# Performance work log

Hardware: AMD Instinct MI355X
Metric: run time of the kernel (lower is better)

The kernel has to match this reference:

```python
import jax, jax.numpy as jnp
import numpy as np

D_MODEL = 768
KERNELS = [7, 5, 3]
FILTERS = [40, 30, 20]
FC_IN = sum(FILTERS)  # 90


def setup_inputs() -> dict:
    key = jax.random.key(0)
    ks = jax.random.split(key, 16)
    B, S, D = 8, 2048, D_MODEL
    inp = {
        'x1': jax.random.normal(ks[0], (B, S, D), jnp.float32),
        'x2': jax.random.normal(ks[1], (B, S, D), jnp.float32),
    }
    # conv weights: OIH layout [out_ch, in_ch, k]
    for i, (k, f) in enumerate(zip(KERNELS, FILTERS)):
        scale = 1.0 / np.sqrt(D * k)
        inp[f'w{k}'] = jax.random.uniform(ks[2 + 2 * i], (f, D, k), jnp.float32, -scale, scale)
        inp[f'b{k}'] = jax.random.uniform(ks[3 + 2 * i], (f,), jnp.float32, -scale, scale)
    inp['U'] = jax.random.normal(ks[8], (D, D), jnp.float32) * (1.0 / np.sqrt(D))
    inp['bias_v'] = jax.random.normal(ks[9], (D,), jnp.float32) * 0.02
    inp['fc_w'] = jax.random.normal(ks[10], (D, FC_IN), jnp.float32) * (1.0 / np.sqrt(FC_IN))
    inp['fc_b'] = jnp.zeros((D,), jnp.float32)
    inp['fcx_w'] = jax.random.normal(ks[11], (D, 2 * D), jnp.float32) * (1.0 / np.sqrt(2 * D))
    inp['fcx_b'] = jnp.zeros((D,), jnp.float32)
    return inp


def _conv1d_same(x_ncs, w_oik, b_o, k):
    # x: [B, C, S], w: [O, C, k] -> [B, O, S], 'same' padding = k//2
    y = jax.lax.conv_general_dilated(
        x_ncs, w_oik, window_strides=(1,), padding=[(k // 2, k // 2)],
        dimension_numbers=('NCH', 'OIH', 'NCH'))
    return y + b_o[None, :, None]


def reference(x1, x2, w7, b7, w5, b5, w3, b3, U, bias_v, fc_w, fc_b, fcx_w, fcx_b):
    # CNN branch over x2 (dropout layers are identity in eval mode)
    xc = jnp.transpose(x2, (0, 2, 1))  # [B, D, S]
    feats = jnp.concatenate([
        jnp.transpose(_conv1d_same(xc, w7, b7, 7), (0, 2, 1)),
        jnp.transpose(_conv1d_same(xc, w5, b5, 5), (0, 2, 1)),
        jnp.transpose(_conv1d_same(xc, w3, b3, 3), (0, 2, 1)),
    ], axis=-1)                                    # [B, S, 90]
    x = jnp.tanh(jax.nn.relu(feats) @ fc_w.T + fc_b)  # [B, S, D]
    # biaffine attention: x1 @ U @ x2^T + x2 @ bias (broadcast over rows)
    attn = jnp.einsum('bsd,de,bte->bst', x1, U, x2) + (x2 @ bias_v)[:, None, :]
    attn = jax.nn.softmax(attn, axis=-1)           # [B, S, S]
    out = jnp.tanh(attn @ x2)                      # [B, S, D]
    x = x + out
    return jnp.concatenate([x1, x], axis=-1) @ fcx_w.T + fcx_b  # [B, S, D]
```

## Files before the change

### kernel.cpp

```cpp
#include <hip/hip_runtime.h>
#include <cmath>

#define D_MODEL 768
#define SEQ 2048
#define BATCH 8
#define FC_PAD 96
#define FC_PAD2 128
#define KCOMB (7 * D_MODEL)
#define KCHUNK 2688

typedef unsigned short ushort_t;
typedef _Float16 half_t;
typedef __attribute__((ext_vector_type(8))) _Float16 f16x8;
typedef __attribute__((ext_vector_type(8))) unsigned short u16x8;
typedef __attribute__((ext_vector_type(4))) unsigned short u16x4;
typedef __attribute__((ext_vector_type(4))) float f32x4;

struct Ptr8 { const ushort_t* p[8]; };

__device__ __forceinline__ ushort_t f2h(float x) {
    half_t h = (half_t)x;
    return __builtin_bit_cast(ushort_t, h);
}
__device__ __forceinline__ float h2f(ushort_t u) {
    return (float)__builtin_bit_cast(half_t, u);
}
__device__ __forceinline__ float fast_tanh(float x) {
    float a = fabsf(x);
    float t = __expf(-2.f * a);
    float r = (1.f - t) / (1.f + t);
    return copysignf(r, x);
}
__device__ __forceinline__ void gload16(const ushort_t* g, ushort_t* lbase) {
    __builtin_amdgcn_global_load_lds((const __attribute__((address_space(1))) void*)g,
                                     (__attribute__((address_space(3))) void*)lbase,
                                     16, 0, 0);
}

__global__ void convert_f16_kernel(const float* __restrict__ src, ushort_t* __restrict__ dst, size_t n4) {
    size_t i = (size_t)blockIdx.x * 256 + threadIdx.x;
    if (i >= n4) return;
    f32x4 x = *(const f32x4*)(src + i * 4);
    u16x4 h;
    #pragma unroll
    for (int j = 0; j < 4; ++j) h[j] = f2h(x[j]);
    *(u16x4*)(dst + i * 4) = h;
}

__global__ void convert_fc_kernel(const float* __restrict__ src, ushort_t* __restrict__ dst) {
    int i = blockIdx.x * 256 + threadIdx.x;
    if (i >= D_MODEL * FC_PAD2) return;
    int o = i / FC_PAD2, j = i - o * FC_PAD2;
    dst[i] = (j < 90) ? f2h(src[o * 90 + j]) : 0;
}

__global__ void convert_ut_kernel(const float* __restrict__ U, ushort_t* __restrict__ dst) {
    int i = blockIdx.x * 256 + threadIdx.x;
    if (i >= D_MODEL * D_MODEL) return;
    int n = i / D_MODEL, k = i - n * D_MODEL;
    dst[i] = f2h(U[(size_t)k * D_MODEL + n]);
}

__global__ void build_wcomb_kernel(const float* __restrict__ w7, const float* __restrict__ b7,
                                   const float* __restrict__ w5, const float* __restrict__ b5,
                                   const float* __restrict__ w3, const float* __restrict__ b3,
                                   ushort_t* __restrict__ Wt, float* __restrict__ bcat) {
    int idx = blockIdx.x * 256 + threadIdx.x;
    const int total = FC_PAD2 * KCOMB;
    if (idx < total) {
        int o = idx / KCOMB, k = idx - o * KCOMB;
        int t = k / D_MODEL, d = k - t * D_MODEL;
        float v = 0.f;
        if (o < 40) {
            v = w7[(size_t)o * (D_MODEL * 7) + d * 7 + t];
        } else if (o < 70) {
            int t5 = t - 1;
            if (t5 >= 0 && t5 < 5) v = w5[(size_t)(o - 40) * (D_MODEL * 5) + d * 5 + t5];
        } else if (o < 90) {
            int t3 = t - 2;
            if (t3 >= 0 && t3 < 3) v = w3[(size_t)(o - 70) * (D_MODEL * 3) + d * 3 + t3];
        }
        Wt[idx] = f2h(v);
    }
    if (idx < FC_PAD2) {
        float bv = 0.f;
        if (idx < 40) bv = b7[idx];
        else if (idx < 70) bv = b5[idx - 40];
        else if (idx < 90) bv = b3[idx - 70];
        bcat[idx] = bv;
    }
}

__global__ void conv_reduce_kernel(const float* __restrict__ P, const float* __restrict__ bcat,
                                   ushort_t* __restrict__ feats) {
    const size_t MT = (size_t)BATCH * SEQ;
    size_t i = (size_t)blockIdx.x * 256 + threadIdx.x;
    if (i >= MT * FC_PAD2) return;
    int col = (int)(i & (FC_PAD2 - 1));
    size_t row = i >> 7;
    float v = 0.f;
    if (col < FC_PAD) {
        size_t idx = row * FC_PAD + col;
        const size_t st = MT * FC_PAD;
        v = P[idx] + P[idx + st] + bcat[col];
        v = fmaxf(v, 0.f);
    }
    feats[i] = f2h(v);
}

__global__ void transpose_f16_kernel(const ushort_t* __restrict__ in, ushort_t* __restrict__ out) {
    __shared__ ushort_t tile[32][40];
    int b = blockIdx.z;
    int s0 = blockIdx.x * 32, d0 = blockIdx.y * 32;
    int tx = threadIdx.x & 31, ty = threadIdx.x >> 5;
    const ushort_t* inb = in + (size_t)b * SEQ * D_MODEL;
    ushort_t* outb = out + (size_t)b * D_MODEL * SEQ;
    #pragma unroll
    for (int i = 0; i < 4; ++i)
        tile[ty + i * 8][tx] = inb[(size_t)(s0 + ty + i * 8) * D_MODEL + d0 + tx];
    __syncthreads();
    #pragma unroll
    for (int i = 0; i < 4; ++i)
        outb[(size_t)(d0 + ty + i * 8) * SEQ + s0 + tx] = tile[tx][ty + i * 8];
}

template<int TM, int TN, int AMODE, int ACT, int HASBIAS, int HASADD,
         int OUTMODE, int KSPLIT, int APTR, int MAP, int ZM, int GX, int GY,
         int SMEPI, int ASCALE>
__global__ __launch_bounds__(256, 3)
void mfma_gemm(const ushort_t* __restrict__ A, const ushort_t* __restrict__ A2,
               const ushort_t* __restrict__ B, const float* __restrict__ bias,
               const ushort_t* __restrict__ addsrc,
               float* __restrict__ Cf, ushort_t* __restrict__ Ch,
               Ptr8 ap, float* __restrict__ smw, float* __restrict__ slw,
               int M, int N, int K, int lda, int ldb, int ldc,
               size_t sA, size_t sB, size_t sBias, size_t sC) {
    constexpr int WM = TM / 2, WN = TN / 2, FM = WM / 16, FN = WN / 16;
    __shared__ __align__(16) ushort_t As_[TM * 64];
    __shared__ __align__(16) ushort_t Bs_[TN * 64];
    __shared__ float pmS[SMEPI ? 4 : 1][SMEPI ? 64 : 1];
    __shared__ float msS[SMEPI ? 128 : 1];
    __shared__ float plS[SMEPI ? 4 : 1][SMEPI ? 64 : 1];
    __shared__ ushort_t alS[ASCALE ? 16 : 1][ASCALE ? 128 : 1];

    int bx, by, z;
    if (MAP == 1) {
        int lin = blockIdx.x;
        z = lin % ZM;
        int t = lin / ZM;
        bx = t % GX;
        by = t / GX;
    } else if (MAP == 2) {
        int lin = blockIdx.x;
        int xcd = lin & 7;
        int t = lin >> 3;
        by = t % GY;
        bx = xcd * (GX / 8) + t / GY;
        z = 0;
    } else if (MAP == 3) {
        int lin = blockIdx.x;
        z = lin % ZM;
        int t = lin / ZM;
        by = t % GY;
        bx = t / GY;
    } else {
        bx = blockIdx.x; by = blockIdx.y; z = blockIdx.z;
    }

    const int kb = KSPLIT ? z * K : 0;
    const ushort_t* Ab = APTR ? ap.p[z] : (A + (KSPLIT ? 0 : (size_t)z * sA));
    const ushort_t* Bb = B + (KSPLIT ? 0 : (size_t)z * sB);
    if (HASBIAS) bias += (size_t)z * sBias;
    if (HASADD) addsrc += (size_t)z * sC;
    if (OUTMODE == 0) Cf += (size_t)z * sC;
    else if (!SMEPI) Ch += (size_t)z * sC;

    const int m0 = bx * TM;
    const int n0 = by * TN;
    const int tid = threadIdx.x;
    const int lane = tid & 63;
    const int wave = tid >> 6;
    const int wm = (wave >> 1) * WM, wn = (wave & 1) * WN;
    const int r16 = lane & 15, kq = lane >> 4;
    const int srow = tid >> 3;
    const int slot = tid & 7;

    if (ASCALE) {
        if (tid < 128) {
            int row = tid;
            int gm = m0 + row;
            float mt[16], al[16];
            float mg = -3.0e38f;
            #pragma unroll
            for (int t = 0; t < 16; ++t) {
                mt[t] = smw[((size_t)z * 16 + t) * SEQ + gm];
                mg = fmaxf(mg, mt[t]);
            }
            float lg = 0.f;
            #pragma unroll
            for (int t = 0; t < 16; ++t) {
                float e = __expf(mt[t] - mg);
                lg += slw[((size_t)z * 16 + t) * SEQ + gm] * e;
                al[t] = e;
            }
            float inv = 1.f / lg;
            #pragma unroll
            for (int t = 0; t < 16; ++t) alS[t][row] = f2h(al[t] * inv);
        }
        __syncthreads();
    }

    f32x4 acc[FM][FN];
    #pragma unroll
    for (int i = 0; i < FM; ++i)
        #pragma unroll
        for (int j = 0; j < FN; ++j) acc[i][j] = (f32x4){0.f, 0.f, 0.f, 0.f};

    const u16x8 zv = {0, 0, 0, 0, 0, 0, 0, 0};

    for (int k0 = 0; k0 < K; k0 += 64) {
        #pragma unroll
        for (int i = 0; i < TM / 32; ++i) {
            int row = i * 32 + srow;
            int gm = m0 + row;
            int xs = slot ^ (row & 7);
            if (AMODE == 1) {
                int gkk = kb + k0 + xs * 8;
                int t = gkk / D_MODEL, d = gkk - t * D_MODEL;
                int s = (gm & (SEQ - 1)) + t - 3;
                int bb = gm >> 11;
                u16x8 v = (s >= 0 && s < SEQ) ? *(const u16x8*)(Ab + ((size_t)(bb * SEQ + s)) * lda + d) : zv;
                *(u16x8*)&As_[(size_t)row * 64 + slot * 8] = v;
            } else {
                const ushort_t* src;
                if (AMODE == 2) {
                    int gk = k0 + xs * 8;
                    src = (gk < D_MODEL) ? Ab + (size_t)gm * D_MODEL + gk
                                         : A2 + (size_t)gm * D_MODEL + (gk - D_MODEL);
                } else {
                    int gk = kb + k0 + xs * 8;
                    src = Ab + (size_t)gm * lda + gk;
                }
                gload16(src, &As_[(size_t)(i * 32 + wave * 8) * 64]);
            }
        }
        #pragma unroll
        for (int i = 0; i < TN / 32; ++i) {
            int row = i * 32 + srow;
            int gn = n0 + row;
            int xs = slot ^ (row & 7);
            int gk = kb + k0 + xs * 8;
            gload16(Bb + (size_t)gn * ldb + gk, &Bs_[(size_t)(i * 32 + wave * 8) * 64]);
        }
        __syncthreads();

        f16x8 ah[FM][2], bh[FN][2];
        #pragma unroll
        for (int mi = 0; mi < FM; ++mi) {
            int row = wm + mi * 16 + r16;
            #pragma unroll
            for (int kk = 0; kk < 2; ++kk)
                ah[mi][kk] = *(const f16x8*)&As_[(size_t)row * 64 + (((kk * 4 + kq) ^ (row & 7)) * 8)];
        }
        if (ASCALE) {
            const int kt = k0 >> 7;
            #pragma unroll
            for (int mi = 0; mi < FM; ++mi) {
                half_t s = __builtin_bit_cast(half_t, alS[kt][wm + mi * 16 + r16]);
                ah[mi][0] = ah[mi][0] * s;
                ah[mi][1] = ah[mi][1] * s;
            }
        }
        #pragma unroll
        for (int ni = 0; ni < FN; ++ni) {
            int row = wn + ni * 16 + r16;
            #pragma unroll
            for (int kk = 0; kk < 2; ++kk)
                bh[ni][kk] = *(const f16x8*)&Bs_[(size_t)row * 64 + (((kk * 4 + kq) ^ (row & 7)) * 8)];
        }
        #pragma unroll
        for (int kk = 0; kk < 2; ++kk)
            #pragma unroll
            for (int mi = 0; mi < FM; ++mi)
                #pragma unroll
                for (int ni = 0; ni < FN; ++ni)
                    acc[mi][ni] = __builtin_amdgcn_mfma_f32_16x16x32_f16(ah[mi][kk], bh[ni][kk], acc[mi][ni], 0, 0, 0);
        __syncthreads();
    }

    if (SMEPI) {
        float pmax[FM][4];
        #pragma unroll
        for (int mi = 0; mi < FM; ++mi)
            #pragma unroll
            for (int r = 0; r < 4; ++r) {
                float mx = -3.0e38f;
                #pragma unroll
                for (int ni = 0; ni < FN; ++ni) {
                    float v = acc[mi][ni][r];
                    if (HASBIAS) { v += bias[n0 + wn + ni * 16 + r16]; acc[mi][ni][r] = v; }
                    mx = fmaxf(mx, v);
                }
                mx = fmaxf(mx, __shfl_xor(mx, 1));
                mx = fmaxf(mx, __shfl_xor(mx, 2));
                mx = fmaxf(mx, __shfl_xor(mx, 4));
                mx = fmaxf(mx, __shfl_xor(mx, 8));
                pmax[mi][r] = mx;
            }
        if (r16 == 0) {
            #pragma unroll
            for (int mi = 0; mi < FM; ++mi)
                #pragma unroll
                for (int r = 0; r < 4; ++r)
                    pmS[wave][mi * 16 + kq * 4 + r] = pmax[mi][r];
        }
        __syncthreads();
        if (tid < 128) {
            int rl = tid & 63, grp = tid >> 6;
            msS[grp * 64 + rl] = fmaxf(pmS[grp * 2][rl], pmS[grp * 2 + 1][rl]);
        }
        __syncthreads();
        #pragma unroll
        for (int mi = 0; mi < FM; ++mi)
            #pragma unroll
            for (int r = 0; r < 4; ++r) {
                float mrow = msS[wm + mi * 16 + kq * 4 + r];
                float s = 0.f;
                #pragma unroll
                for (int ni = 0; ni < FN; ++ni) {
                    float e = __expf(acc[mi][ni][r] - mrow);
                    acc[mi][ni][r] = e;
                    s += e;
                }
                s += __shfl_xor(s, 1);
                s += __shfl_xor(s, 2);
                s += __shfl_xor(s, 4);
                s += __shfl_xor(s, 8);
                pmax[mi][r] = s;
            }
        if (r16 == 0) {
            #pragma unroll
            for (int mi = 0; mi < FM; ++mi)
                #pragma unroll
                for (int r = 0; r < 4; ++r)
                    plS[wave][mi * 16 + kq * 4 + r] = pmax[mi][r];
        }
        __syncthreads();
        if (tid < 128) {
            int rl = tid & 63, grp = tid >> 6;
            int row = grp * 64 + rl;
            float l2 = plS[grp * 2][rl] + plS[grp * 2 + 1][rl];
            size_t si = ((size_t)z * 16 + by) * SEQ + (m0 + row);
            smw[si] = msS[row];
            slw[si] = l2;
        }
        ushort_t* Co = (ushort_t*)ap.p[z];
        #pragma unroll
        for (int mi = 0; mi < FM; ++mi)
            #pragma unroll
            for (int ni = 0; ni < FN; ++ni)
                #pragma unroll
                for (int r = 0; r < 4; ++r) {
                    int gm = m0 + wm + mi * 16 + kq * 4 + r;
                    int gn = n0 + wn + ni * 16 + r16;
                    Co[(size_t)gm * SEQ + gn] = f2h(acc[mi][ni][r]);
                }
        return;
    }

    #pragma unroll
    for (int mi = 0; mi < FM; ++mi)
        #pragma unroll
        for (int ni = 0; ni < FN; ++ni)
            #pragma unroll
            for (int r = 0; r < 4; ++r) {
                int gm = m0 + wm + mi * 16 + kq * 4 + r;
                int gn = n0 + wn + ni * 16 + r16;
                if (gn >= N) continue;
                float v = acc[mi][ni][r];
                if (HASBIAS) v += bias[gn];
                if (ACT == 1) v = fmaxf(v, 0.f);
                else if (ACT == 2) v = fast_tanh(v);
                if (HASADD) v += h2f(addsrc[(size_t)gm * ldc + gn]);
                size_t idx = (size_t)gm * ldc + gn;
                if (OUTMODE == 0) Cf[idx] = v;
                else Ch[idx] = f2h(v);
            }
}

extern "C" void kernel_launch(void* const* d_in, const int* in_sizes, int n_in,
                              void* d_out, int out_size, void* d_ws, size_t ws_size,
                              hipStream_t stream) {
    const float* x1     = (const float*)d_in[0];
    const float* x2     = (const float*)d_in[1];
    const float* w7     = (const float*)d_in[2];
    const float* b7     = (const float*)d_in[3];
    const float* w5     = (const float*)d_in[4];
    const float* b5     = (const float*)d_in[5];
    const float* w3     = (const float*)d_in[6];
    const float* b3     = (const float*)d_in[7];
    const float* U      = (const float*)d_in[8];
    const float* bias_v = (const float*)d_in[9];
    const float* fc_w   = (const float*)d_in[10];
    const float* fc_b   = (const float*)d_in[11];
    const float* fcx_w  = (const float*)d_in[12];
    const float* fcx_b  = (const float*)d_in[13];
    float* out = (float*)d_out;

    const size_t MT = (size_t)BATCH * SEQ;
    const size_t NE = MT * D_MODEL;
    const size_t NEb = (size_t)SEQ * D_MODEL;
    const size_t SEGSZ = (size_t)SEQ * SEQ;

    char* p = (char*)d_ws;
    auto alloc = [&](size_t bytes) -> char* {
        char* r = p;
        p += (bytes + 255) & ~(size_t)255;
        return r;
    };
    ushort_t* x1_h   = (ushort_t*)alloc(NE * 2);
    ushort_t* x2_h   = (ushort_t*)alloc(NE * 2);
    ushort_t* x2t    = (ushort_t*)alloc(NE * 2);
    ushort_t* y1     = (ushort_t*)alloc(NE * 2);
    ushort_t* xcnn   = (ushort_t*)alloc(NE * 2);
    float*    convp  = (float*)   alloc(MT * FC_PAD * 4 * 4);
    ushort_t* feats  = (ushort_t*)alloc(MT * FC_PAD2 * 2);
    ushort_t* Wt     = (ushort_t*)alloc((size_t)FC_PAD2 * KCOMB * 2);
    ushort_t* fc_wt  = (ushort_t*)alloc((size_t)D_MODEL * FC_PAD2 * 2);
    ushort_t* fcx_wt = (ushort_t*)alloc((size_t)D_MODEL * 2 * D_MODEL * 2);
    ushort_t* Ut     = (ushort_t*)alloc((size_t)D_MODEL * D_MODEL * 2);
    float*    bcat   = (float*)alloc(FC_PAD2 * 4);
    float*    smS    = (float*)alloc((size_t)BATCH * 16 * SEQ * 4);
    float*    slS    = (float*)alloc((size_t)BATCH * 16 * SEQ * 4);

    ushort_t* dob = (ushort_t*)d_out;
    Ptr8 ap;
    ap.p[0] = (ushort_t*)convp;
    ap.p[1] = (ushort_t*)convp + SEGSZ;
    ap.p[2] = (ushort_t*)convp + 2 * SEGSZ;
    ap.p[3] = dob;
    ap.p[4] = dob + SEGSZ;
    ap.p[5] = dob + 2 * SEGSZ;
    ap.p[6] = dob + 3 * SEGSZ;
    ap.p[7] = dob + 4 * SEGSZ;
    Ptr8 apz = {};

    const int T = 256;
    auto blk = [](size_t n) { return dim3((unsigned)((n + 255) / 256)); };

    build_wcomb_kernel<<<blk((size_t)FC_PAD2 * KCOMB), T, 0, stream>>>(w7, b7, w5, b5, w3, b3, Wt, bcat);
    convert_fc_kernel<<<blk((size_t)D_MODEL * FC_PAD2), T, 0, stream>>>(fc_w, fc_wt);
    convert_f16_kernel<<<blk((size_t)D_MODEL * 2 * D_MODEL / 4), T, 0, stream>>>(fcx_w, fcx_wt, (size_t)D_MODEL * 2 * D_MODEL / 4);
    convert_ut_kernel<<<blk((size_t)D_MODEL * D_MODEL), T, 0, stream>>>(U, Ut);
    convert_f16_kernel<<<blk(NE / 4), T, 0, stream>>>(x1, x1_h, NE / 4);
    convert_f16_kernel<<<blk(NE / 4), T, 0, stream>>>(x2, x2_h, NE / 4);
    transpose_f16_kernel<<<dim3(SEQ / 32, D_MODEL / 32, BATCH), T, 0, stream>>>(x2_h, x2t);

    mfma_gemm<64, 128, 1, 0, 0, 0, 0, 1, 0, 0, 1, 1, 1, 0, 0><<<dim3(MT / 64, 1, 2), T, 0, stream>>>(
        x2_h, nullptr, Wt, nullptr, nullptr,
        convp, nullptr, apz, nullptr, nullptr,
        (int)MT, FC_PAD, KCHUNK, D_MODEL, KCOMB, FC_PAD,
        0, 0, 0, MT * FC_PAD);
    conv_reduce_kernel<<<blk(MT * FC_PAD2), T, 0, stream>>>(convp, bcat, feats);

    mfma_gemm<128, 128, 0, 2, 1, 0, 1, 0, 0, 2, 1, 128, 6, 0, 0><<<dim3(768, 1, 1), T, 0, stream>>>(
        feats, nullptr, fc_wt, fc_b, nullptr,
        nullptr, xcnn, apz, nullptr, nullptr,
        (int)MT, D_MODEL, FC_PAD2, FC_PAD2, FC_PAD2, D_MODEL, 0, 0, 0, 0);

    mfma_gemm<128, 128, 0, 0, 1, 0, 1, 0, 0, 2, 1, 128, 6, 0, 0><<<dim3(768, 1, 1), T, 0, stream>>>(
        x1_h, nullptr, Ut, bias_v, nullptr,
        nullptr, y1, apz, nullptr, nullptr,
        (int)MT, D_MODEL, D_MODEL, D_MODEL, D_MODEL, D_MODEL, 0, 0, 0, 0);

    mfma_gemm<128, 128, 0, 0, 0, 0, 1, 0, 0, 1, 8, 16, 16, 1, 0><<<dim3(2048, 1, 1), T, 0, stream>>>(
        y1, nullptr, x2_h, nullptr, nullptr,
        nullptr, nullptr, ap, smS, slS,
        SEQ, SEQ, D_MODEL, D_MODEL, D_MODEL, SEQ,
        NEb, NEb, 0, 0);

    mfma_gemm<128, 128, 0, 2, 0, 1, 1, 0, 1, 3, 8, 16, 6, 0, 1><<<dim3(768, 1, 1), T, 0, stream>>>(
        nullptr, nullptr, x2t, nullptr,
        xcnn,
        nullptr, xcnn, ap, smS, slS,
        SEQ, D_MODEL, SEQ, SEQ, SEQ, D_MODEL,
        0, NEb, 0, NEb);

    mfma_gemm<128, 128, 2, 0, 1, 0, 0, 0, 0, 2, 1, 128, 6, 0, 0><<<dim3(768, 1, 1), T, 0, stream>>>(
        x1_h, xcnn, fcx_wt, fcx_b, nullptr,
        out, nullptr, apz, nullptr, nullptr,
        (int)MT, D_MODEL, 2 * D_MODEL, D_MODEL, 2 * D_MODEL, D_MODEL, 0, 0, 0, 0);
}
```

Before: 340.0 us.

## Merge weight-prep kernels, fuse x2 conversion with transpose, raise occupancy bound

Combines four weight conversion kernels into a single prep launch and fuses the x2 fp32-to-fp16 conversion with its transpose, so x2 is read once and the intermediate f16 re-read disappears. The goal is fewer launches and less memory traffic in the preprocessing stage. It also raises the GEMM launch bounds from 3 to 4 waves per SIMD, which may force register spilling in the heavy GEMMs. The fused transpose writes f16 scalars, so its global stores are narrower.

```diff
diff --git a/kernel.cpp b/kernel.cpp
--- a/kernel.cpp
+++ b/kernel.cpp
@@ -47,27 +47,42 @@
     *(u16x4*)(dst + i * 4) = h;
 }
 
-__global__ void convert_fc_kernel(const float* __restrict__ src, ushort_t* __restrict__ dst) {
-    int i = blockIdx.x * 256 + threadIdx.x;
-    if (i >= D_MODEL * FC_PAD2) return;
-    int o = i / FC_PAD2, j = i - o * FC_PAD2;
-    dst[i] = (j < 90) ? f2h(src[o * 90 + j]) : 0;
-}
-
-__global__ void convert_ut_kernel(const float* __restrict__ U, ushort_t* __restrict__ dst) {
-    int i = blockIdx.x * 256 + threadIdx.x;
-    if (i >= D_MODEL * D_MODEL) return;
-    int n = i / D_MODEL, k = i - n * D_MODEL;
-    dst[i] = f2h(U[(size_t)k * D_MODEL + n]);
-}
-
-__global__ void build_wcomb_kernel(const float* __restrict__ w7, const float* __restrict__ b7,
-                                   const float* __restrict__ w5, const float* __restrict__ b5,
-                                   const float* __restrict__ w3, const float* __restrict__ b3,
-                                   ushort_t* __restrict__ Wt, float* __restrict__ bcat) {
+__global__ void convert_x2_kernel(const float* __restrict__ in,
+                                  ushort_t* __restrict__ x2h, ushort_t* __restrict__ x2t) {
+    __shared__ ushort_t tile[32][33];
+    int b = blockIdx.z;
+    int s0 = blockIdx.x * 32, d0 = blockIdx.y * 32;
+    int tx = threadIdx.x & 31, ty = threadIdx.x >> 5;
+    const float* inb = in + (size_t)b * SEQ * D_MODEL;
+    ushort_t* hb = x2h + (size_t)b * SEQ * D_MODEL;
+    ushort_t* tb = x2t + (size_t)b * D_MODEL * SEQ;
+    #pragma unroll
+    for (int i = 0; i < 4; ++i) {
+        int s = s0 + ty + i * 8;
+        ushort_t h = f2h(inb[(size_t)s * D_MODEL + d0 + tx]);
+        hb[(size_t)s * D_MODEL + d0 + tx] = h;
+        tile[ty + i * 8][tx] = h;
+    }
+    __syncthreads();
+    #pragma unroll
+    for (int i = 0; i < 4; ++i)
+        tb[(size_t)(d0 + ty + i * 8) * SEQ + s0 + tx] = tile[tx][ty + i * 8];
+}
+
+#define R0 (FC_PAD2 * KCOMB)
+#define R1 (D_MODEL * FC_PAD2)
+#define R2 (D_MODEL * 2 * D_MODEL)
+#define R3 (D_MODEL * D_MODEL)
+__global__ void prep_weights_kernel(const float* __restrict__ w7, const float* __restrict__ b7,
+                                    const float* __restrict__ w5, const float* __restrict__ b5,
+                                    const float* __restrict__ w3, const float* __restrict__ b3,
+                                    const float* __restrict__ fc_w, const float* __restrict__ fcx_w,
+                                    const float* __restrict__ U,
+                                    ushort_t* __restrict__ Wt, ushort_t* __restrict__ fc_wt,
+                                    ushort_t* __restrict__ fcx_wt, ushort_t* __restrict__ Ut,
+                                    float* __restrict__ bcat) {
     int idx = blockIdx.x * 256 + threadIdx.x;
-    const int total = FC_PAD2 * KCOMB;
-    if (idx < total) {
+    if (idx < R0) {
         int o = idx / KCOMB, k = idx - o * KCOMB;
         int t = k / D_MODEL, d = k - t * D_MODEL;
         float v = 0.f;
@@ -81,7 +96,26 @@
             if (t3 >= 0 && t3 < 3) v = w3[(size_t)(o - 70) * (D_MODEL * 3) + d * 3 + t3];
         }
         Wt[idx] = f2h(v);
-    }
+        return;
+    }
+    idx -= R0;
+    if (idx < R1) {
+        int o = idx / FC_PAD2, j = idx - o * FC_PAD2;
+        fc_wt[idx] = (j < 90) ? f2h(fc_w[o * 90 + j]) : 0;
+        return;
+    }
+    idx -= R1;
+    if (idx < R2) {
+        fcx_wt[idx] = f2h(fcx_w[idx]);
+        return;
+    }
+    idx -= R2;
+    if (idx < R3) {
+        int n = idx / D_MODEL, k = idx - n * D_MODEL;
+        Ut[idx] = f2h(U[(size_t)k * D_MODEL + n]);
+        return;
+    }
+    idx -= R3;
     if (idx < FC_PAD2) {
         float bv = 0.f;
         if (idx < 40) bv = b7[idx];
@@ -108,26 +142,10 @@
     feats[i] = f2h(v);
 }
 
-__global__ void transpose_f16_kernel(const ushort_t* __restrict__ in, ushort_t* __restrict__ out) {
-    __shared__ ushort_t tile[32][40];
-    int b = blockIdx.z;
-    int s0 = blockIdx.x * 32, d0 = blockIdx.y * 32;
-    int tx = threadIdx.x & 31, ty = threadIdx.x >> 5;
-    const ushort_t* inb = in + (size_t)b * SEQ * D_MODEL;
-    ushort_t* outb = out + (size_t)b * D_MODEL * SEQ;
-    #pragma unroll
-    for (int i = 0; i < 4; ++i)
-        tile[ty + i * 8][tx] = inb[(size_t)(s0 + ty + i * 8) * D_MODEL + d0 + tx];
-    __syncthreads();
-    #pragma unroll
-    for (int i = 0; i < 4; ++i)
-        outb[(size_t)(d0 + ty + i * 8) * SEQ + s0 + tx] = tile[tx][ty + i * 8];
-}
-
 template<int TM, int TN, int AMODE, int ACT, int HASBIAS, int HASADD,
          int OUTMODE, int KSPLIT, int APTR, int MAP, int ZM, int GX, int GY,
          int SMEPI, int ASCALE>
-__global__ __launch_bounds__(256, 3)
+__global__ __launch_bounds__(256, 4)
 void mfma_gemm(const ushort_t* __restrict__ A, const ushort_t* __restrict__ A2,
                const ushort_t* __restrict__ B, const float* __restrict__ bias,
                const ushort_t* __restrict__ addsrc,
@@ -448,13 +466,10 @@
     const int T = 256;
     auto blk = [](size_t n) { return dim3((unsigned)((n + 255) / 256)); };
 
-    build_wcomb_kernel<<<blk((size_t)FC_PAD2 * KCOMB), T, 0, stream>>>(w7, b7, w5, b5, w3, b3, Wt, bcat);
-    convert_fc_kernel<<<blk((size_t)D_MODEL * FC_PAD2), T, 0, stream>>>(fc_w, fc_wt);
-    convert_f16_kernel<<<blk((size_t)D_MODEL * 2 * D_MODEL / 4), T, 0, stream>>>(fcx_w, fcx_wt, (size_t)D_MODEL * 2 * D_MODEL / 4);
-    convert_ut_kernel<<<blk((size_t)D_MODEL * D_MODEL), T, 0, stream>>>(U, Ut);
+    prep_weights_kernel<<<blk((size_t)R0 + R1 + R2 + R3 + FC_PAD2), T, 0, stream>>>(
+        w7, b7, w5, b5, w3, b3, fc_w, fcx_w, U, Wt, fc_wt, fcx_wt, Ut, bcat);
     convert_f16_kernel<<<blk(NE / 4), T, 0, stream>>>(x1, x1_h, NE / 4);
-    convert_f16_kernel<<<blk(NE / 4), T, 0, stream>>>(x2, x2_h, NE / 4);
-    transpose_f16_kernel<<<dim3(SEQ / 32, D_MODEL / 32, BATCH), T, 0, stream>>>(x2_h, x2t);
+    convert_x2_kernel<<<dim3(SEQ / 32, D_MODEL / 32, BATCH), T, 0, stream>>>(x2, x2_h, x2t);
 
     mfma_gemm<64, 128, 1, 0, 0, 0, 0, 1, 0, 0, 1, 1, 1, 0, 0><<<dim3(MT / 64, 1, 2), T, 0, stream>>>(
         x2_h, nullptr, Wt, nullptr, nullptr,
```

Result: faster. 329.8 us (median of 2 runs) (-3.0%).
